# Optimization experiments

Measured on AMD Instinct MI355X. Metric: run time of the kernel, lower is better.

## Reference

```python
import jax, jax.numpy as jnp
import numpy as np
import math

B, L, E, H = 4, 1024, 1024, 16
D = E // H  # head_dim = 64
SCALE = 8.0
EPS = 1e-6

def setup_inputs() -> dict:
    key = jax.random.key(0)
    ks = jax.random.split(key, 16)
    def xavier(k, shape):
        fan_in, fan_out = shape[1], shape[0]
        a = math.sqrt(6.0 / (fan_in + fan_out))
        return jax.random.uniform(k, shape, jnp.float32, -a, a)
    return {
        "query": jax.random.normal(ks[0], (B, L, E), jnp.float32),
        "key": jax.random.normal(ks[1], (B, L, E), jnp.float32),
        "value": jax.random.normal(ks[2], (B, L, E), jnp.float32),
        "attn_mask": jax.random.uniform(ks[3], (B, L), jnp.float32),
        "key_padding_mask": jax.random.randint(ks[4], (B, L), 0, 2) > 0,
        "Wq": xavier(ks[5], (E, E)), "bq": jnp.zeros((E,), jnp.float32),
        "Wk": xavier(ks[6], (E, E)), "bk": jnp.zeros((E,), jnp.float32),
        "Wv": xavier(ks[7], (E, E)), "bv": jnp.zeros((E,), jnp.float32),
        "Wo": xavier(ks[8], (E, E)), "bo": jnp.zeros((E,), jnp.float32),
    }

def reference(query, key, value, attn_mask, key_padding_mask,
              Wq, bq, Wk, bk, Wv, bv, Wo, bo):
    # projections (torch Linear: x @ W.T + b)
    q = (query @ Wq.T + bq).reshape(B, L, H, D).transpose(0, 2, 1, 3)  # (B,H,L,D)
    k = (key @ Wk.T + bk).reshape(B, L, H, D).transpose(0, 2, 1, 3)
    v = (value @ Wv.T + bv).reshape(B, L, H, D).transpose(0, 2, 1, 3)
    scores = jnp.einsum('bhqd,bhkd->bhqk', q, k) / math.sqrt(D)  # (B,H,L,L)
    # soft log-mask bias (training path: no hard -inf at mask==0)
    log_mask = jnp.log(jnp.clip(attn_mask, EPS))  # (B,L)
    scores = scores + SCALE * log_mask[:, None, None, :]
    # key padding mask -> -inf
    scores = jnp.where(key_padding_mask[:, None, None, :], -jnp.inf, scores)
    attn_weights = jax.nn.softmax(scores, axis=-1)  # dropout p=0 -> identity
    attn_output = jnp.einsum('bhqk,bhkd->bhqd', attn_weights, v)
    attn_output = attn_output.transpose(0, 2, 1, 3).reshape(B, L, E)
    attn_output = attn_output @ Wo.T + bo
    return attn_output, attn_weights.mean(axis=1)
```

## Files before the change

kernel.cpp:

```cpp
#include <hip/hip_runtime.h>
#include <math.h>

#define Bsz 4
#define Lq  1024
#define Emb 1024
#define Hh  16
#define Dd  64

typedef short bf16x8 __attribute__((ext_vector_type(8)));
typedef float f32x4 __attribute__((ext_vector_type(4)));

static __device__ __forceinline__ unsigned short f2bf(float f) {
    unsigned u = __float_as_uint(f);
    return (unsigned short)((u + 0x7FFFu + ((u >> 16) & 1u)) >> 16);
}
static __device__ __forceinline__ unsigned pack2(float lo, float hi) {
    return __builtin_amdgcn_perm(__float_as_uint(hi) + 0x8000u,
                                 __float_as_uint(lo) + 0x8000u, 0x07060302u);
}

static __device__ __forceinline__ float cross_max(float x) {
    x = fmaxf(x, __shfl_xor(x, 16, 64));
    x = fmaxf(x, __shfl_xor(x, 32, 64));
    return x;
}
static __device__ __forceinline__ float cross_sum(float x) {
    x += __shfl_xor(x, 16, 64);
    x += __shfl_xor(x, 32, 64);
    return x;
}

#define GLOAD_LDS16(gp, lp) __builtin_amdgcn_global_load_lds(                  \
    (const __attribute__((address_space(1))) void*)(gp),                       \
    (__attribute__((address_space(3))) void*)(lp), 16, 0, 0)

__global__ __launch_bounds__(256) void cvt_all(const float* __restrict__ q,
                                               const float* __restrict__ k,
                                               const float* __restrict__ v,
                                               const float* __restrict__ w0,
                                               const float* __restrict__ w1,
                                               const float* __restrict__ w2,
                                               const float* __restrict__ w3,
                                               unsigned short* __restrict__ qo,
                                               unsigned short* __restrict__ ko,
                                               unsigned short* __restrict__ vo,
                                               unsigned short* __restrict__ o0,
                                               unsigned short* __restrict__ o1,
                                               unsigned short* __restrict__ o2,
                                               unsigned short* __restrict__ o3,
                                               const float* __restrict__ mask,
                                               const int* __restrict__ kpm,
                                               float* __restrict__ bias)
{
    if (blockIdx.x >= 16384) {
        int i = (blockIdx.x - 16384) * 256 + threadIdx.x;
        float bv = 8.0f * logf(fmaxf(mask[i], 1e-6f));
        bias[i] = kpm[i] ? -INFINITY : bv;
        return;
    }
    int i = blockIdx.x * 256 + threadIdx.x;
    const float* src; unsigned short* dst; int off;
    if (i < 1048576)      { src = q; dst = qo; off = i; }
    else if (i < 2097152) { src = k; dst = ko; off = i - 1048576; }
    else if (i < 3145728) { src = v; dst = vo; off = i - 2097152; }
    else {
        int j = i - 3145728;
        int reg = j >> 18; off = j & 262143;
        src = (reg == 0) ? w0 : (reg == 1) ? w1 : (reg == 2) ? w2 : w3;
        dst = (reg == 0) ? o0 : (reg == 1) ? o1 : (reg == 2) ? o2 : o3;
    }
    float4 x = ((const float4*)src)[off];
    ushort4 o;
    o.x = f2bf(x.x); o.y = f2bf(x.y); o.z = f2bf(x.z); o.w = f2bf(x.w);
    ((ushort4*)dst)[off] = o;
}

__global__ __launch_bounds__(256) void gemm_qkv(const unsigned short* __restrict__ Aq,
                                                const unsigned short* __restrict__ Ak,
                                                const unsigned short* __restrict__ Av,
                                                const unsigned short* __restrict__ Wq,
                                                const unsigned short* __restrict__ Wk,
                                                const unsigned short* __restrict__ Wv,
                                                const float* __restrict__ biq,
                                                const float* __restrict__ bik,
                                                const float* __restrict__ biv,
                                                unsigned short* __restrict__ Oq,
                                                unsigned short* __restrict__ Ok,
                                                unsigned short* __restrict__ Ov)
{
    const int K = 1024;
    __shared__ unsigned short sA[2][64][64];
    __shared__ unsigned short sB[2][128][64];
    int tid = threadIdx.x;
    int w = tid >> 6, lane = tid & 63;

    int bid = blockIdx.x;
    int which = bid >> 9;
    int lin = bid & 511;
    int xcd = lin & 7, idx = lin >> 3;
    int bm = (xcd * 8 + (idx >> 3)) * 64;
    int bn = (idx & 7) * 128;

    const unsigned short* A = (which == 0) ? Aq : (which == 1) ? Ak : Av;
    const unsigned short* Bw = (which == 0) ? Wq : (which == 1) ? Wk : Wv;
    const float* bias = (which == 0) ? biq : (which == 1) ? bik : biv;
    unsigned short* outp = (which == 0) ? Oq : (which == 1) ? Ok : Ov;

    int wr = (w >> 1) * 32, wc = (w & 1) * 64;
    int fr = lane & 15, fg = lane >> 4;
    int csw = fr & 7;

    int srl = lane >> 3;
    int scb = (lane & 7) ^ srl;

    const unsigned short* Ag = A + (size_t)(bm + w * 16 + srl) * K + scb * 8;
    const unsigned short* Bg = Bw + (size_t)(bn + w * 32 + srl) * K + scb * 8;

#define STAGE(BUF, K0) do {                                                      \
    _Pragma("unroll")                                                            \
    for (int j = 0; j < 2; ++j)                                                  \
        GLOAD_LDS16(Ag + (size_t)j * 8 * K + (K0), &sA[BUF][w * 16 + j * 8][0]); \
    _Pragma("unroll")                                                            \
    for (int j = 0; j < 4; ++j)                                                  \
        GLOAD_LDS16(Bg + (size_t)j * 8 * K + (K0), &sB[BUF][w * 32 + j * 8][0]); \
} while (0)

    f32x4 acc[2][4];
#pragma unroll
    for (int i = 0; i < 2; ++i)
#pragma unroll
        for (int j = 0; j < 4; ++j) acc[i][j] = (f32x4){0.f, 0.f, 0.f, 0.f};

    STAGE(0, 0);
    __syncthreads();

#pragma unroll 1
    for (int k0 = 0; k0 < K; k0 += 64) {
        int cur = (k0 >> 6) & 1;
        if (k0 + 64 < K) STAGE(cur ^ 1, k0 + 64);
        bf16x8 af[2][2], bfv[4][2];
#pragma unroll
        for (int i = 0; i < 2; ++i)
#pragma unroll
            for (int kk = 0; kk < 2; ++kk)
                af[i][kk] = *(const bf16x8*)&sA[cur][wr + i * 16 + fr][((kk * 4 + fg) ^ csw) * 8];
#pragma unroll
        for (int j = 0; j < 4; ++j)
#pragma unroll
            for (int kk = 0; kk < 2; ++kk)
                bfv[j][kk] = *(const bf16x8*)&sB[cur][wc + j * 16 + fr][((kk * 4 + fg) ^ csw) * 8];
#pragma unroll
        for (int i = 0; i < 2; ++i)
#pragma unroll
            for (int j = 0; j < 4; ++j) {
                acc[i][j] = __builtin_amdgcn_mfma_f32_16x16x32_bf16(af[i][0], bfv[j][0], acc[i][j], 0, 0, 0);
                acc[i][j] = __builtin_amdgcn_mfma_f32_16x16x32_bf16(af[i][1], bfv[j][1], acc[i][j], 0, 0, 0);
            }
        __syncthreads();
    }
#undef STAGE

    int rb = (lane >> 4) * 4;
#pragma unroll
    for (int j = 0; j < 4; ++j) {
        int n = bn + wc + j * 16 + fr;
        float bia = bias[n];
#pragma unroll
        for (int i = 0; i < 2; ++i) {
#pragma unroll
            for (int r = 0; r < 4; ++r) {
                int m = bm + wr + i * 16 + rb + r;
                float v = acc[i][j][r] + bia;
                int b = m >> 10, l = m & 1023, h = n >> 6, d = n & 63;
                if (which == 2)
                    outp[(((size_t)(b * Hh + h)) * Dd + d) * Lq + l] = f2bf(v);
                else
                    outp[(((size_t)(b * Hh + h)) * Lq + l) * Dd + d] = f2bf(v);
            }
        }
    }
}

__global__ __launch_bounds__(256) void attn_flash(const unsigned short* __restrict__ Qh,
                                                  const unsigned short* __restrict__ Kh,
                                                  const unsigned short* __restrict__ Vt,
                                                  const float* __restrict__ mbias,
                                                  unsigned short* __restrict__ ctx,
                                                  float* __restrict__ mstats,
                                                  float* __restrict__ lstats)
{
    __shared__ float sBias[1024];
    __shared__ unsigned short Wl[4][2][16][64];
    __shared__ unsigned short Kl[2][64][64];
    __shared__ unsigned short Vl[2][64][64];

    int tid = threadIdx.x;
    int w = tid >> 6, lane = tid & 63;
    int fr = lane & 15, fg = lane >> 4;

    int lin = blockIdx.x;
    int xcd = lin & 7, jj = lin >> 3;
    int pair = xcd * 8 + (jj >> 3);
    int qt = jj & 7;
    int b = pair & 3, h = pair >> 2;

    int q0A = qt * 128 + w * 32;
    int q0B = q0A + 16;
    int swz = (fr & 7) << 2;
    int csw = fr & 7;

    const unsigned short* Qp = Qh + ((size_t)(b * Hh + h)) * Lq * Dd;
    const unsigned short* Kp = Kh + ((size_t)(b * Hh + h)) * Lq * Dd;
    const unsigned short* Vp = Vt + ((size_t)(b * Hh + h)) * Dd * Lq;

    int srl = lane >> 3;
    int scb = (lane & 7) ^ srl;

#define STAGEK(BUF, KC) do {                                                     \
    _Pragma("unroll")                                                            \
    for (int i = 0; i < 2; ++i)                                                  \
        GLOAD_LDS16(Kp + (size_t)((KC) + w * 16 + i * 8 + srl) * Dd + scb * 8,   \
                    &Kl[BUF][w * 16 + i * 8][0]);                                \
} while (0)
#define STAGEV(BUF, KC) do {                                                     \
    _Pragma("unroll")                                                            \
    for (int i = 0; i < 2; ++i)                                                  \
        GLOAD_LDS16(Vp + (size_t)(w * 16 + i * 8 + srl) * Lq + (KC) + scb * 8,   \
                    &Vl[BUF][w * 16 + i * 8][0]);                                \
} while (0)

    for (int i = tid; i < 1024; i += 256) sBias[i] = mbias[b * Lq + i];

    bf16x8 qA0 = *(const bf16x8*)(Qp + (size_t)(q0A + fr) * Dd + fg * 8);
    bf16x8 qA1 = *(const bf16x8*)(Qp + (size_t)(q0A + fr) * Dd + 32 + fg * 8);
    bf16x8 qB0 = *(const bf16x8*)(Qp + (size_t)(q0B + fr) * Dd + fg * 8);
    bf16x8 qB1 = *(const bf16x8*)(Qp + (size_t)(q0B + fr) * Dd + 32 + fg * 8);

    f32x4 OA[4], OB[4];
#pragma unroll
    for (int dt = 0; dt < 4; ++dt) { OA[dt] = (f32x4){0.f,0.f,0.f,0.f}; OB[dt] = (f32x4){0.f,0.f,0.f,0.f}; }
    float mA = -INFINITY, lsA = 0.f, mB = -INFINITY, lsB = 0.f;

    bf16x8 vb0[4], vb1[4];

#define RDK(K0, K1, BUF) do {                                                    \
    _Pragma("unroll")                                                            \
    for (int kt = 0; kt < 4; ++kt) {                                             \
        K0[kt] = *(const bf16x8*)&Kl[BUF][kt * 16 + fr][(fg ^ csw) * 8];         \
        K1[kt] = *(const bf16x8*)&Kl[BUF][kt * 16 + fr][((4 + fg) ^ csw) * 8];   \
    }                                                                            \
} while (0)
#define RDV(BUF) do {                                                            \
    _Pragma("unroll")                                                            \
    for (int dt = 0; dt < 4; ++dt) {                                             \
        vb0[dt] = *(const bf16x8*)&Vl[BUF][dt * 16 + fr][(fg ^ csw) * 8];        \
        vb1[dt] = *(const bf16x8*)&Vl[BUF][dt * 16 + fr][((4 + fg) ^ csw) * 8];  \
    }                                                                            \
} while (0)

#define QK(S, K0, K1, B0, B1) do {                                               \
    _Pragma("unroll")                                                            \
    for (int kt = 0; kt < 4; ++kt) {                                             \
        S[kt] = __builtin_amdgcn_mfma_f32_16x16x32_bf16(K0[kt], B0, (f32x4){0.f,0.f,0.f,0.f}, 0, 0, 0); \
        S[kt] = __builtin_amdgcn_mfma_f32_16x16x32_bf16(K1[kt], B1, S[kt], 0, 0, 0); \
    }                                                                            \
} while (0)

#define SMPV(S, MT, LS, OT, TI, KC) do {                                         \
    float v_[16];                                                                \
    _Pragma("unroll")                                                            \
    for (int kt = 0; kt < 4; ++kt) {                                             \
        float4 bb = *(const float4*)&sBias[(KC) + kt * 16 + fg * 4];             \
        _Pragma("unroll")                                                        \
        for (int r = 0; r < 4; ++r)                                              \
            v_[kt * 4 + r] = S[kt][r] * 0.125f + (&bb.x)[r];                     \
    }                                                                            \
    float t8[8];                                                                 \
    _Pragma("unroll")                                                            \
    for (int i = 0; i < 8; ++i) t8[i] = fmaxf(v_[i], v_[i + 8]);                 \
    float t4[4];                                                                 \
    _Pragma("unroll")                                                            \
    for (int i = 0; i < 4; ++i) t4[i] = fmaxf(t8[i], t8[i + 4]);                 \
    float pmax = fmaxf(fmaxf(t4[0], t4[1]), fmaxf(t4[2], t4[3]));                \
    pmax = cross_max(pmax);                                                      \
    float mn = fmaxf(MT, pmax);                                                  \
    float sc = __expf(MT - mn);                                                  \
    _Pragma("unroll")                                                            \
    for (int i = 0; i < 16; ++i) v_[i] = __expf(v_[i] - mn);                     \
    _Pragma("unroll")                                                            \
    for (int i = 0; i < 8; ++i) t8[i] = v_[i] + v_[i + 8];                       \
    _Pragma("unroll")                                                            \
    for (int i = 0; i < 4; ++i) t4[i] = t8[i] + t8[i + 4];                       \
    LS = LS * sc + (t4[0] + t4[1]) + (t4[2] + t4[3]);                            \
    MT = mn;                                                                     \
    _Pragma("unroll")                                                            \
    for (int dt = 0; dt < 4; ++dt)                                               \
        _Pragma("unroll")                                                        \
        for (int r = 0; r < 4; ++r) OT[dt][r] *= sc;                             \
    _Pragma("unroll")                                                            \
    for (int kt = 0; kt < 4; ++kt) {                                             \
        unsigned w0 = pack2(v_[kt * 4 + 0], v_[kt * 4 + 1]);                     \
        unsigned w1 = pack2(v_[kt * 4 + 2], v_[kt * 4 + 3]);                     \
        uint2 pr; pr.x = w0; pr.y = w1;                                          \
        *(uint2*)&Wl[w][TI][fr][2 * ((kt * 8 + fg * 2) ^ swz)] = pr;             \
    }                                                                            \
    bf16x8 pa0 = *(const bf16x8*)&Wl[w][TI][fr][2 * ((fg * 4) ^ swz)];           \
    bf16x8 pa1 = *(const bf16x8*)&Wl[w][TI][fr][2 * ((16 + fg * 4) ^ swz)];      \
    _Pragma("unroll")                                                            \
    for (int dt = 0; dt < 4; ++dt) {                                             \
        OT[dt] = __builtin_amdgcn_mfma_f32_16x16x32_bf16(vb0[dt], pa0, OT[dt], 0, 0, 0); \
        OT[dt] = __builtin_amdgcn_mfma_f32_16x16x32_bf16(vb1[dt], pa1, OT[dt], 0, 0, 0); \
    }                                                                            \
} while (0)

    STAGEK(0, 0);
    STAGEV(0, 0);
    __syncthreads();

#pragma unroll 1
    for (int c = 0; c < 16; ++c) {
        int cur = c & 1;
        if (c < 15) {
            STAGEK(cur ^ 1, (c + 1) * 64);
            STAGEV(cur ^ 1, (c + 1) * 64);
        }
        bf16x8 k0[4], k1[4];
        RDK(k0, k1, cur);
        f32x4 SA[4], SB[4];
        QK(SA, k0, k1, qA0, qA1);
        QK(SB, k0, k1, qB0, qB1);
        RDV(cur);
        SMPV(SA, mA, lsA, OA, 0, c * 64);
        SMPV(SB, mB, lsB, OB, 1, c * 64);
        __syncthreads();
    }
#undef STAGEK
#undef STAGEV
#undef RDK
#undef RDV
#undef QK
#undef SMPV

    float lAt = cross_sum(lsA), lBt = cross_sum(lsB);
    float liA = 1.f / lAt, liB = 1.f / lBt;
#pragma unroll
    for (int dt = 0; dt < 4; ++dt) {
#pragma unroll
        for (int r = 0; r < 4; ++r) { OA[dt][r] *= liA; OB[dt][r] *= liB; }
    }
#pragma unroll
    for (int dt = 0; dt < 4; ++dt) {
        uint2 pa; pa.x = pack2(OA[dt][0], OA[dt][1]); pa.y = pack2(OA[dt][2], OA[dt][3]);
        *(uint2*)(ctx + ((size_t)(b * Lq + q0A + fr)) * Emb + h * Dd + dt * 16 + fg * 4) = pa;
        uint2 pb; pb.x = pack2(OB[dt][0], OB[dt][1]); pb.y = pack2(OB[dt][2], OB[dt][3]);
        *(uint2*)(ctx + ((size_t)(b * Lq + q0B + fr)) * Emb + h * Dd + dt * 16 + fg * 4) = pb;
    }

    if (lane < 16) {
        mstats[(size_t)(b * Hh + h) * Lq + q0A + lane] = mA;
        lstats[(size_t)(b * Hh + h) * Lq + q0A + lane] = liA;
        mstats[(size_t)(b * Hh + h) * Lq + q0B + lane] = mB;
        lstats[(size_t)(b * Hh + h) * Lq + q0B + lane] = liB;
    }
}

__global__ __launch_bounds__(256) void tail_fused(const unsigned short* __restrict__ A,
                                                  const unsigned short* __restrict__ Bw,
                                                  const float* __restrict__ bias,
                                                  float* __restrict__ outp,
                                                  const unsigned short* __restrict__ Qh,
                                                  const unsigned short* __restrict__ Kh,
                                                  const float* __restrict__ mbias,
                                                  const float* __restrict__ mstats,
                                                  const float* __restrict__ lstats,
                                                  float* __restrict__ out2)
{
    __shared__ char smem[49152];
    const int K = 1024;
    int tid = threadIdx.x;
    int w = tid >> 6, lane = tid & 63;
    int fr = lane & 15, fg = lane >> 4;
    int csw = fr & 7;
    int srl = lane >> 3;
    int scb = (lane & 7) ^ srl;

    if (blockIdx.x < 512) {
        unsigned short (*sA)[64][64]  = (unsigned short(*)[64][64])smem;
        unsigned short (*sB)[128][64] = (unsigned short(*)[128][64])(smem + 16384);

        int lin = blockIdx.x;
        int xcd = lin & 7, idx = lin >> 3;
        int bm = (xcd * 8 + (idx >> 3)) * 64;
        int bn = (idx & 7) * 128;
        int wr = (w >> 1) * 32, wc = (w & 1) * 64;

        const unsigned short* Ag = A + (size_t)(bm + w * 16 + srl) * K + scb * 8;
        const unsigned short* Bg = Bw + (size_t)(bn + w * 32 + srl) * K + scb * 8;

#define STAGE_O(BUF, K0) do {                                                    \
    _Pragma("unroll")                                                            \
    for (int j = 0; j < 2; ++j)                                                  \
        GLOAD_LDS16(Ag + (size_t)j * 8 * K + (K0), &sA[BUF][w * 16 + j * 8][0]); \
    _Pragma("unroll")                                                            \
    for (int j = 0; j < 4; ++j)                                                  \
        GLOAD_LDS16(Bg + (size_t)j * 8 * K + (K0), &sB[BUF][w * 32 + j * 8][0]); \
} while (0)

        f32x4 acc[2][4];
#pragma unroll
        for (int i = 0; i < 2; ++i)
#pragma unroll
            for (int j = 0; j < 4; ++j) acc[i][j] = (f32x4){0.f, 0.f, 0.f, 0.f};

        STAGE_O(0, 0);
        __syncthreads();

#pragma unroll 1
        for (int k0 = 0; k0 < K; k0 += 64) {
            int cur = (k0 >> 6) & 1;
            if (k0 + 64 < K) STAGE_O(cur ^ 1, k0 + 64);
            bf16x8 af[2][2], bfv[4][2];
#pragma unroll
            for (int i = 0; i < 2; ++i)
#pragma unroll
                for (int kk = 0; kk < 2; ++kk)
                    af[i][kk] = *(const bf16x8*)&sA[cur][wr + i * 16 + fr][((kk * 4 + fg) ^ csw) * 8];
#pragma unroll
            for (int j = 0; j < 4; ++j)
#pragma unroll
                for (int kk = 0; kk < 2; ++kk)
                    bfv[j][kk] = *(const bf16x8*)&sB[cur][wc + j * 16 + fr][((kk * 4 + fg) ^ csw) * 8];
#pragma unroll
            for (int i = 0; i < 2; ++i)
#pragma unroll
                for (int j = 0; j < 4; ++j) {
                    acc[i][j] = __builtin_amdgcn_mfma_f32_16x16x32_bf16(af[i][0], bfv[j][0], acc[i][j], 0, 0, 0);
                    acc[i][j] = __builtin_amdgcn_mfma_f32_16x16x32_bf16(af[i][1], bfv[j][1], acc[i][j], 0, 0, 0);
                }
            __syncthreads();
        }
#undef STAGE_O

        int rb = (lane >> 4) * 4;
#pragma unroll
        for (int j = 0; j < 4; ++j) {
            int n = bn + wc + j * 16 + fr;
            float bia = bias[n];
#pragma unroll
            for (int i = 0; i < 2; ++i)
#pragma unroll
                for (int r = 0; r < 4; ++r) {
                    int m = bm + wr + i * 16 + rb + r;
                    outp[(size_t)m * 1024 + n] = acc[i][j][r] + bia;
                }
        }
    } else {
        unsigned short (*sQ)[32][64]  = (unsigned short(*)[32][64])smem;
        unsigned short (*sK)[128][64] = (unsigned short(*)[128][64])(smem + 8192);
        float (*sM)[32]  = (float(*)[32])(smem + 40960);
        float (*sLi)[32] = (float(*)[32])(smem + 43008);

        int bid = blockIdx.x - 512;
        int q0 = (bid & 31) * 32;
        int kc = ((bid >> 5) & 7) * 128;
        int b  = bid >> 8;

        for (int i = tid; i < 512; i += 256) {
            int h = i >> 5, qq = i & 31;
            sM[h][qq]  = mstats[(size_t)(b * Hh + h) * Lq + q0 + qq];
            sLi[h][qq] = lstats[(size_t)(b * Hh + h) * Lq + q0 + qq];
        }

#define STAGEH(BUF, H) do {                                                      \
    const unsigned short* Qp_ = Qh + ((size_t)(b * Hh + (H))) * Lq * Dd;         \
    const unsigned short* Kp_ = Kh + ((size_t)(b * Hh + (H))) * Lq * Dd;         \
    GLOAD_LDS16(Qp_ + (size_t)(q0 + w * 8 + srl) * Dd + scb * 8, &sQ[BUF][w * 8][0]); \
    _Pragma("unroll")                                                            \
    for (int i = 0; i < 4; ++i)                                                  \
        GLOAD_LDS16(Kp_ + (size_t)(kc + w * 32 + i * 8 + srl) * Dd + scb * 8,    \
                    &sK[BUF][w * 32 + i * 8][0]);                                \
} while (0)

#define RDH(AQ, BKk, BUF) do {                                                   \
    _Pragma("unroll")                                                            \
    for (int rt = 0; rt < 2; ++rt)                                               \
        _Pragma("unroll")                                                        \
        for (int ks = 0; ks < 2; ++ks)                                           \
            AQ[rt][ks] = *(const bf16x8*)&sQ[BUF][rt * 16 + fr][((ks * 4 + fg) ^ csw) * 8]; \
    _Pragma("unroll")                                                            \
    for (int ct = 0; ct < 2; ++ct)                                               \
        _Pragma("unroll")                                                        \
        for (int ks = 0; ks < 2; ++ks)                                           \
            BKk[ct][ks] = *(const bf16x8*)&sK[BUF][w * 32 + ct * 16 + fr][((ks * 4 + fg) ^ csw) * 8]; \
} while (0)

#define COMPH(AQ, BKk, H) do {                                                   \
    float4 mrow[2], lirow[2];                                                    \
    _Pragma("unroll")                                                            \
    for (int rt = 0; rt < 2; ++rt) {                                             \
        mrow[rt]  = *(const float4*)&sM[(H)][rt * 16 + fg * 4];                  \
        lirow[rt] = *(const float4*)&sLi[(H)][rt * 16 + fg * 4];                 \
    }                                                                            \
    _Pragma("unroll")                                                            \
    for (int rt = 0; rt < 2; ++rt)                                               \
        _Pragma("unroll")                                                        \
        for (int ct = 0; ct < 2; ++ct) {                                         \
            f32x4 s_ = __builtin_amdgcn_mfma_f32_16x16x32_bf16(AQ[rt][0], BKk[ct][0], (f32x4){0.f,0.f,0.f,0.f}, 0, 0, 0); \
            s_ = __builtin_amdgcn_mfma_f32_16x16x32_bf16(AQ[rt][1], BKk[ct][1], s_, 0, 0, 0); \
            float bia = ct ? bias1 : bias0;                                      \
            _Pragma("unroll")                                                    \
            for (int r = 0; r < 4; ++r)                                          \
                o2[rt][ct][r] += __expf(s_[r] * 0.125f + bia - mrow[rt][r]) * lirow[rt][r]; \
        }                                                                        \
} while (0)

        float bias0 = mbias[b * Lq + kc + w * 32 + fr];
        float bias1 = mbias[b * Lq + kc + w * 32 + 16 + fr];

        float o2[2][2][4];
#pragma unroll
        for (int rt = 0; rt < 2; ++rt)
#pragma unroll
            for (int ct = 0; ct < 2; ++ct)
#pragma unroll
                for (int r = 0; r < 4; ++r) o2[rt][ct][r] = 0.f;

        STAGEH(0, 0);
        __syncthreads();

#pragma unroll 1
        for (int h = 0; h < Hh; ++h) {
            int cur = h & 1;
            if (h < Hh - 1) STAGEH(cur ^ 1, h + 1);
            bf16x8 aq[2][2], bk[2][2];
            RDH(aq, bk, cur);
            COMPH(aq, bk, h);
            __syncthreads();
        }
#undef STAGEH
#undef RDH
#undef COMPH

#pragma unroll
        for (int rt = 0; rt < 2; ++rt)
#pragma unroll
            for (int ct = 0; ct < 2; ++ct)
#pragma unroll
                for (int r = 0; r < 4; ++r)
                    out2[((size_t)(b * Lq + q0 + rt * 16 + fg * 4 + r)) * Lq + kc + w * 32 + ct * 16 + fr]
                        = o2[rt][ct][r] * 0.0625f;
    }
}

extern "C" void kernel_launch(void* const* d_in, const int* in_sizes, int n_in,
                              void* d_out, int out_size, void* d_ws, size_t ws_size,
                              hipStream_t stream)
{
    const float* query = (const float*)d_in[0];
    const float* key   = (const float*)d_in[1];
    const float* value = (const float*)d_in[2];
    const float* amask = (const float*)d_in[3];
    const int*   kpm   = (const int*)d_in[4];
    const float* Wq = (const float*)d_in[5];
    const float* bq = (const float*)d_in[6];
    const float* Wk = (const float*)d_in[7];
    const float* bk = (const float*)d_in[8];
    const float* Wv = (const float*)d_in[9];
    const float* bv = (const float*)d_in[10];
    const float* Wo = (const float*)d_in[11];
    const float* bo = (const float*)d_in[12];

    float* out1 = (float*)d_out;
    float* out2 = out1 + (size_t)Bsz * Lq * Emb;

    const size_t MB = 1u << 20;
    char* ws = (char*)d_ws;
    unsigned short* qbf = (unsigned short*)(ws + 0 * MB);
    unsigned short* kbf = (unsigned short*)(ws + 8 * MB);
    unsigned short* vbf = (unsigned short*)(ws + 16 * MB);
    unsigned short* wqb = (unsigned short*)(ws + 24 * MB);
    unsigned short* wkb = (unsigned short*)(ws + 26 * MB);
    unsigned short* wvb = (unsigned short*)(ws + 28 * MB);
    unsigned short* wob = (unsigned short*)(ws + 30 * MB);
    unsigned short* QhB = (unsigned short*)(ws + 32 * MB);
    unsigned short* KhB = (unsigned short*)(ws + 40 * MB);
    unsigned short* VtB = (unsigned short*)(ws + 48 * MB);
    unsigned short* ctxB = (unsigned short*)(ws + 56 * MB);
    float* mbias  = (float*)(ws + 64 * MB);
    float* mstats = (float*)(ws + 0 * MB);
    float* lstats = (float*)(ws + 0 * MB + 256 * 1024);

    cvt_all<<<16400, 256, 0, stream>>>(query, key, value, Wq, Wk, Wv, Wo,
                                       qbf, kbf, vbf, wqb, wkb, wvb, wob,
                                       amask, kpm, mbias);

    gemm_qkv<<<1536, 256, 0, stream>>>(qbf, kbf, vbf, wqb, wkb, wvb,
                                       bq, bk, bv, QhB, KhB, VtB);

    attn_flash<<<512, 256, 0, stream>>>(QhB, KhB, VtB, mbias, ctxB, mstats, lstats);

    tail_fused<<<1536, 256, 0, stream>>>(ctxB, wob, bo, out1,
                                         QhB, KhB, mbias, mstats, lstats, out2);
}
```

Measured before the change: 143.4 us.

## Split attention over two key halves and merge partials in a combine kernel

The flash attention kernel now launches twice as many blocks, each covering half of the key sequence, and writes unnormalized fp32 partial outputs together with per-row max and sum. A new combine kernel rescales and merges the two partials, writes the bf16 context, and writes the softmax stats consumed by the tail kernel. The aim is better occupancy across the GPU's compute units, since 512 blocks underfill the device. The cost is an extra launch and fp32 partial traffic; one partial buffer reuses the out2 region before tail_fused overwrites it.

```diff
diff --git a/kernel.cpp b/kernel.cpp
--- a/kernel.cpp
+++ b/kernel.cpp
@@ -185,9 +185,12 @@
                                                   const unsigned short* __restrict__ Kh,
                                                   const unsigned short* __restrict__ Vt,
                                                   const float* __restrict__ mbias,
-                                                  unsigned short* __restrict__ ctx,
-                                                  float* __restrict__ mstats,
-                                                  float* __restrict__ lstats)
+                                                  float* __restrict__ pO0,
+                                                  float* __restrict__ pO1,
+                                                  float* __restrict__ mp0,
+                                                  float* __restrict__ lp0,
+                                                  float* __restrict__ mp1,
+                                                  float* __restrict__ lp1)
 {
     __shared__ float sBias[1024];
     __shared__ unsigned short Wl[4][2][16][64];
@@ -199,10 +202,17 @@
     int fr = lane & 15, fg = lane >> 4;
 
     int lin = blockIdx.x;
-    int xcd = lin & 7, jj = lin >> 3;
+    int s = lin >> 9;
+    int rest = lin & 511;
+    int xcd = rest & 7, jj = rest >> 3;
     int pair = xcd * 8 + (jj >> 3);
     int qt = jj & 7;
     int b = pair & 3, h = pair >> 2;
+    int c0 = s * 8;
+
+    float* pO = s ? pO1 : pO0;
+    float* mp = s ? mp1 : mp0;
+    float* lp = s ? lp1 : lp0;
 
     int q0A = qt * 128 + w * 32;
     int q0B = q0A + 16;
@@ -313,14 +323,14 @@
     }                                                                            \
 } while (0)
 
-    STAGEK(0, 0);
-    STAGEV(0, 0);
+    STAGEK(0, c0 * 64);
+    STAGEV(0, c0 * 64);
     __syncthreads();
 
 #pragma unroll 1
-    for (int c = 0; c < 16; ++c) {
-        int cur = c & 1;
-        if (c < 15) {
+    for (int c = c0; c < c0 + 8; ++c) {
+        int cur = (c - c0) & 1;
+        if (c < c0 + 7) {
             STAGEK(cur ^ 1, (c + 1) * 64);
             STAGEV(cur ^ 1, (c + 1) * 64);
         }
@@ -342,26 +352,51 @@
 #undef SMPV
 
     float lAt = cross_sum(lsA), lBt = cross_sum(lsB);
-    float liA = 1.f / lAt, liB = 1.f / lBt;
+
+    size_t bh1024 = (size_t)(b * Hh + h) * Lq;
 #pragma unroll
     for (int dt = 0; dt < 4; ++dt) {
-#pragma unroll
-        for (int r = 0; r < 4; ++r) { OA[dt][r] *= liA; OB[dt][r] *= liB; }
-    }
-#pragma unroll
-    for (int dt = 0; dt < 4; ++dt) {
-        uint2 pa; pa.x = pack2(OA[dt][0], OA[dt][1]); pa.y = pack2(OA[dt][2], OA[dt][3]);
-        *(uint2*)(ctx + ((size_t)(b * Lq + q0A + fr)) * Emb + h * Dd + dt * 16 + fg * 4) = pa;
-        uint2 pb; pb.x = pack2(OB[dt][0], OB[dt][1]); pb.y = pack2(OB[dt][2], OB[dt][3]);
-        *(uint2*)(ctx + ((size_t)(b * Lq + q0B + fr)) * Emb + h * Dd + dt * 16 + fg * 4) = pb;
-    }
-
+        *(f32x4*)(pO + (bh1024 + q0A + fr) * 64 + dt * 16 + fg * 4) = OA[dt];
+        *(f32x4*)(pO + (bh1024 + q0B + fr) * 64 + dt * 16 + fg * 4) = OB[dt];
+    }
     if (lane < 16) {
-        mstats[(size_t)(b * Hh + h) * Lq + q0A + lane] = mA;
-        lstats[(size_t)(b * Hh + h) * Lq + q0A + lane] = liA;
-        mstats[(size_t)(b * Hh + h) * Lq + q0B + lane] = mB;
-        lstats[(size_t)(b * Hh + h) * Lq + q0B + lane] = liB;
-    }
+        mp[bh1024 + q0A + lane] = mA;
+        lp[bh1024 + q0A + lane] = lAt;
+        mp[bh1024 + q0B + lane] = mB;
+        lp[bh1024 + q0B + lane] = lBt;
+    }
+}
+
+__global__ __launch_bounds__(256) void attn_combine(const float* __restrict__ pO0,
+                                                    const float* __restrict__ pO1,
+                                                    const float* __restrict__ mp0,
+                                                    const float* __restrict__ lp0,
+                                                    const float* __restrict__ mp1,
+                                                    const float* __restrict__ lp1,
+                                                    unsigned short* __restrict__ ctx,
+                                                    float* __restrict__ mstats,
+                                                    float* __restrict__ lstats)
+{
+    int i = blockIdx.x * 256 + threadIdx.x;
+    int t4 = i * 4;
+    int row = t4 >> 6, d0 = t4 & 63;
+    float m0 = mp0[row], m1 = mp1[row];
+    float l0 = lp0[row], l1 = lp1[row];
+    float m = fmaxf(m0, m1);
+    float w0 = __expf(m0 - m), w1 = __expf(m1 - m);
+    float li = 1.f / (l0 * w0 + l1 * w1);
+    float4 a = ((const float4*)pO0)[i];
+    float4 bq = ((const float4*)pO1)[i];
+    float o0 = (a.x * w0 + bq.x * w1) * li;
+    float o1 = (a.y * w0 + bq.y * w1) * li;
+    float o2v = (a.z * w0 + bq.z * w1) * li;
+    float o3 = (a.w * w0 + bq.w * w1) * li;
+    int q = row & 1023, bh = row >> 10;
+    int b = bh >> 4, h = bh & 15;
+    ushort4 ov;
+    ov.x = f2bf(o0); ov.y = f2bf(o1); ov.z = f2bf(o2v); ov.w = f2bf(o3);
+    *(ushort4*)(ctx + ((size_t)(b * Lq + q)) * Emb + h * Dd + d0) = ov;
+    if (d0 == 0) { mstats[row] = m; lstats[row] = li; }
 }
 
 __global__ __launch_bounds__(256) void tail_fused(const unsigned short* __restrict__ A,
@@ -587,8 +622,15 @@
     unsigned short* VtB = (unsigned short*)(ws + 48 * MB);
     unsigned short* ctxB = (unsigned short*)(ws + 56 * MB);
     float* mbias  = (float*)(ws + 64 * MB);
-    float* mstats = (float*)(ws + 0 * MB);
-    float* lstats = (float*)(ws + 0 * MB + 256 * 1024);
+
+    float* pO0 = (float*)(ws + 0 * MB);
+    float* pO1 = out2;
+    float* mp0 = (float*)(ws + 16 * MB);
+    float* lp0 = (float*)(ws + 16 * MB + 256 * 1024);
+    float* mp1 = (float*)(ws + 16 * MB + 512 * 1024);
+    float* lp1 = (float*)(ws + 16 * MB + 768 * 1024);
+    float* mstats = (float*)(ws + 17 * MB);
+    float* lstats = (float*)(ws + 17 * MB + 256 * 1024);
 
     cvt_all<<<16400, 256, 0, stream>>>(query, key, value, Wq, Wk, Wv, Wo,
                                        qbf, kbf, vbf, wqb, wkb, wvb, wob,
@@ -597,7 +639,10 @@
     gemm_qkv<<<1536, 256, 0, stream>>>(qbf, kbf, vbf, wqb, wkb, wvb,
                                        bq, bk, bv, QhB, KhB, VtB);
 
-    attn_flash<<<512, 256, 0, stream>>>(QhB, KhB, VtB, mbias, ctxB, mstats, lstats);
+    attn_flash<<<1024, 256, 0, stream>>>(QhB, KhB, VtB, mbias,
+                                         pO0, pO1, mp0, lp0, mp1, lp1);
+    attn_combine<<<4096, 256, 0, stream>>>(pO0, pO1, mp0, lp0, mp1, lp1,
+                                           ctxB, mstats, lstats);
 
     tail_fused<<<1536, 256, 0, stream>>>(ctxB, wob, bo, out1,
                                          QhB, KhB, mbias, mstats, lstats, out2);
```

New measurement: 154.1 us. 7.5% more time.
